# Optimization experiments

Hardware: AMD Instinct MI355X
Metric: run time of the kernel (lower is better)

The kernel has to match this reference:

```python
import jax, jax.numpy as jnp
import numpy as np

D_MODEL = 1024
NUM_HEADS = 16
D_K = D_MODEL // NUM_HEADS
LN_EPS = 1e-5
NEG = -1e9


def setup_inputs() -> dict:
    key = jax.random.key(0)
    ks = jax.random.split(key, 12)
    B, S, D = 8, 1024, D_MODEL
    lim = 1.0 / np.sqrt(D)
    def lin(k):
        k1, k2 = jax.random.split(k)
        W = jax.random.uniform(k1, (D, D), jnp.float32, -lim, lim)
        b = jax.random.uniform(k2, (D,), jnp.float32, -lim, lim)
        return W, b
    Wq, bq = lin(ks[0])
    Wk, bk = lin(ks[1])
    Wv, bv = lin(ks[2])
    Wo, bo = lin(ks[3])
    return {
        "history_items": jax.random.normal(ks[4], (B, S, D), jnp.float32),
        "sequence_mask": jax.random.randint(ks[5], (B, S), 0, 2, jnp.int32),
        "Wq": Wq, "bq": bq, "Wk": Wk, "bk": bk,
        "Wv": Wv, "bv": bv, "Wo": Wo, "bo": bo,
        "ln_gamma": jnp.ones((D,), jnp.float32),
        "ln_beta": jnp.zeros((D,), jnp.float32),
    }


def reference(history_items, sequence_mask, Wq, bq, Wk, bk, Wv, bv, Wo, bo, ln_gamma, ln_beta):
    B, S, D = history_items.shape
    H, dk = NUM_HEADS, D_K
    # projections -> [B, H, S, dk]
    def proj(W, b):
        return (history_items @ W.T + b).reshape(B, S, H, dk).transpose(0, 2, 1, 3)
    q = proj(Wq, bq)
    k = proj(Wk, bk)
    v = proj(Wv, bv)
    # combined mask: causal [1,1,S,S] AND key-padding [B,1,1,S]
    causal = jnp.tril(jnp.ones((S, S), bool))[None, None]
    mask = jnp.logical_and(causal, (sequence_mask != 0)[:, None, None, :])
    scores = jnp.einsum('bhqd,bhkd->bhqk', q, k) / np.sqrt(dk).astype(np.float32)
    scores = jnp.where(mask, scores, NEG)
    attn = jax.nn.softmax(scores, axis=-1)
    ctx = jnp.einsum('bhqk,bhkd->bhqd', attn, v)  # [B,H,S,dk]
    concat = ctx.transpose(0, 2, 1, 3).reshape(B, S, D)
    out = concat @ Wo.T + bo
    x = out + history_items
    mu = jnp.mean(x, axis=-1, keepdims=True)
    var = jnp.mean((x - mu) ** 2, axis=-1, keepdims=True)
    return (x - mu) * jax.lax.rsqrt(var + LN_EPS) * ln_gamma + ln_beta
```

## Files before the change

### kernel.cpp

```cpp
#include <hip/hip_runtime.h>
#include <hip/hip_bf16.h>

#define B_ 8
#define S_ 1024
#define D_ 1024
#define H_ 16
#define DK_ 64
#define M_ (B_*S_)

#define QSCALE 0.1803368801111904f

typedef __attribute__((ext_vector_type(4))) float f32x4;
typedef __attribute__((ext_vector_type(8))) short bf16x8;
typedef __attribute__((ext_vector_type(4))) short s16x4;
typedef __hip_bfloat16 bf16;
typedef unsigned long long ull;

#define GLOAD_LDS16(gp, lp) __builtin_amdgcn_global_load_lds( \
    (const __attribute__((address_space(1))) void*)(gp), \
    (__attribute__((address_space(3))) void*)(lp), 16, 0, 0)

#define SBAR()   asm volatile("s_barrier" ::: "memory")
#define VMCNT(n) asm volatile("s_waitcnt vmcnt(" #n ")" ::: "memory")

__device__ __forceinline__ bf16x8 ld8(const bf16* p){ return *(const bf16x8*)p; }

__device__ __forceinline__ short bf16bits(float f){
  bf16 h = __float2bfloat16(f);
  return __builtin_bit_cast(short, h);
}
__device__ __forceinline__ float tof(short b){
  unsigned u = ((unsigned)(unsigned short)b) << 16;
  return __builtin_bit_cast(float, u);
}

__device__ __forceinline__ bf16x8 ld8swz(const bf16* base, int row, int colb){
  int sw = colb ^ ((row & 7) << 4);
  return *(const bf16x8*)((const char*)base + row*128 + sw);
}

template<int CTRL>
__device__ __forceinline__ float dppadd(float x){
  int m = __builtin_amdgcn_update_dpp(0, __builtin_bit_cast(int,x), CTRL, 0xF, 0xF, true);
  return x + __builtin_bit_cast(float,m);
}
__device__ __forceinline__ float red16add(float x){
  x = dppadd<0xB1>(x);
  x = dppadd<0x4E>(x);
  x = dppadd<0x141>(x);
  x = dppadd<0x140>(x);
  return x;
}

__global__ __launch_bounds__(256) void cast_f32_bf16(const float* __restrict__ in,
                                                     bf16* __restrict__ out, int n){
  int i = (blockIdx.x*256 + threadIdx.x)*8;
  if (i >= n) return;
  f32x4 a = *(const f32x4*)(in+i);
  f32x4 b = *(const f32x4*)(in+i+4);
  bf16x8 o;
  #pragma unroll
  for (int c=0;c<4;c++){ o[c] = bf16bits(a[c]); o[c+4] = bf16bits(b[c]); }
  *(bf16x8*)(out+i) = o;
}

__global__ __launch_bounds__(256) void cast_w4(const float* __restrict__ w0, const float* __restrict__ w1,
                                               const float* __restrict__ w2, const float* __restrict__ w3,
                                               bf16* __restrict__ out){
  int sel = blockIdx.x >> 9;
  const float* src = (sel==0)?w0:((sel==1)?w1:((sel==2)?w2:w3));
  int i = (((blockIdx.x & 511)*256) + threadIdx.x)*8;
  f32x4 a = *(const f32x4*)(src+i);
  f32x4 b = *(const f32x4*)(src+i+4);
  bf16x8 o;
  #pragma unroll
  for (int c=0;c<4;c++){ o[c] = bf16bits(a[c]); o[c+4] = bf16bits(b[c]); }
  *(bf16x8*)(out + ((size_t)sel<<20) + i) = o;
}

__global__ __launch_bounds__(256) void vmean_kernel(const bf16* __restrict__ Vt_g,
                                                    float* __restrict__ vmean){
  int r = blockIdx.x*4 + (threadIdx.x>>6);
  int lane = threadIdx.x & 63;
  const bf16* p = Vt_g + (((size_t)r)<<10) + lane*16;
  bf16x8 a = ld8(p), c = ld8(p+8);
  float s = 0.f;
  #pragma unroll
  for (int e=0;e<8;e++) s += tof(a[e]) + tof(c[e]);
  #pragma unroll
  for (int off=1;off<64;off<<=1) s += __shfl_xor(s, off);
  if (lane==0) vmean[r] = s * (1.f/1024.f);
}

template<int MODE>
__global__ __launch_bounds__(256) void gemm128(
    const bf16* __restrict__ A,
    const bf16* __restrict__ W0, const bf16* __restrict__ W1, const bf16* __restrict__ W2,
    const float* __restrict__ b0, const float* __restrict__ b1, const float* __restrict__ b2,
    bf16* __restrict__ o0, bf16* __restrict__ o1, bf16* __restrict__ o2,
    const float* __restrict__ resid, float* __restrict__ xout)
{
  const bf16* Wsel = W0; const float* bsel = b0;
  if (MODE==0){
    int z = blockIdx.z;
    Wsel = (z==0)?W0:((z==1)?W1:W2);
    bsel = (z==0)?b0:((z==1)?b1:b2);
  }
  __shared__ bf16 smem[4*128*64];
  const int tid = threadIdx.x, wid = tid>>6, lane = tid&63;
  const int lr = lane&15, lg = lane>>4;
  const int m0 = blockIdx.x*128, n0 = blockIdx.y*128;
  const int wr = wid>>1, wc = wid&1;
  f32x4 acc[4][4] = {};

  auto STAGE = [&](int k0, int bsel_){
    #pragma unroll
    for (int c=0;c<4;c++){
      int ldsoff = ((c<<2)|wid)<<10;
      int off = ldsoff + (lane<<4);
      int row = off>>7;
      int colb = (off&127) ^ ((row&7)<<4);
      GLOAD_LDS16(A   + (((size_t)(m0+row))<<10) + k0 + (colb>>1), (char*)smem + bsel_*32768 + ldsoff);
      GLOAD_LDS16(Wsel+ (((size_t)(n0+row))<<10) + k0 + (colb>>1), (char*)smem + bsel_*32768 + 16384 + ldsoff);
    }
  };

  STAGE(0, 0);
  int cur = 0;
  for (int kt=0; kt<16; kt++){
    if (kt < 15){ STAGE((kt+1)<<6, cur^1); VMCNT(8); }
    else        { VMCNT(0); }
    SBAR();
    __builtin_amdgcn_sched_barrier(0);
    const bf16* Asb = smem + cur*16384;
    const bf16* Bsb = Asb + 8192;
    bf16x8 af[4][2], bfv[4][2];
    #pragma unroll
    for (int m=0;m<4;m++){
      int row = wr*64 + m*16 + lr;
      af[m][0] = ld8swz(Asb, row, lg*16);
      af[m][1] = ld8swz(Asb, row, lg*16 + 64);
    }
    #pragma unroll
    for (int n=0;n<4;n++){
      int row = wc*64 + n*16 + lr;
      bfv[n][0] = ld8swz(Bsb, row, lg*16);
      bfv[n][1] = ld8swz(Bsb, row, lg*16 + 64);
    }
    #pragma unroll
    for (int m=0;m<4;m++)
      #pragma unroll
      for (int n=0;n<4;n++){
        acc[m][n] = __builtin_amdgcn_mfma_f32_16x16x32_bf16(af[m][0], bfv[n][0], acc[m][n],0,0,0);
        acc[m][n] = __builtin_amdgcn_mfma_f32_16x16x32_bf16(af[m][1], bfv[n][1], acc[m][n],0,0,0);
      }
    __builtin_amdgcn_sched_barrier(0);
    SBAR();
    cur ^= 1;
  }

  if (MODE==0){
    if (blockIdx.z == 2){
      __syncthreads();
      #pragma unroll
      for (int n=0;n<4;n++){
        int c = wc*64 + n*16 + lr;
        float bias = bsel[n0 + c];
        #pragma unroll
        for (int m=0;m<4;m++){
          int r0 = wr*64 + m*16 + lg*4;
          s16x4 pk;
          #pragma unroll
          for (int j=0;j<4;j++) pk[j] = bf16bits(acc[m][n][j] + bias);
          *(s16x4*)((char*)smem + c*256 + ((r0*2) ^ ((c&7)<<4))) = pk;
        }
      }
      __syncthreads();
      #pragma unroll
      for (int q=0;q<8;q++){
        int idx = tid + q*256;
        int c = idx>>4, r8 = idx&15;
        bf16x8 vv = *(const bf16x8*)((char*)smem + c*256 + ((r8*16) ^ ((c&7)<<4)));
        int col = n0 + c;  int h = col>>6, dd = col&63;
        int row0 = m0 + r8*8;  int bb = row0>>10, s0 = row0&1023;
        *(bf16x8*)(o2 + ((((size_t)bb*H_ + h)*DK_ + dd)<<10) + s0) = vv;
      }
    } else {
      bf16* osel = (blockIdx.z==0) ? o0 : o1;
      const float qs = (blockIdx.z==0) ? QSCALE : 1.0f;
      #pragma unroll
      for (int n=0;n<4;n++){
        int col = n0 + wc*64 + n*16 + lr;
        float bias = bsel[col];
        int h = col>>6, dd = col&63;
        #pragma unroll
        for (int m=0;m<4;m++)
          #pragma unroll
          for (int j=0;j<4;j++){
            int row = m0 + wr*64 + m*16 + lg*4 + j;
            int bb = row>>10, s = row&1023;
            osel[((((size_t)bb*H_ + h)<<10) + s)*DK_ + dd] = __float2bfloat16((acc[m][n][j] + bias)*qs);
          }
      }
    }
  } else {
    #pragma unroll
    for (int n=0;n<4;n++){
      int col = n0 + wc*64 + n*16 + lr;
      float bias = bsel[col];
      #pragma unroll
      for (int m=0;m<4;m++)
        #pragma unroll
        for (int j=0;j<4;j++){
          int row = m0 + wr*64 + m*16 + lg*4 + j;
          size_t idx = (((size_t)row)<<10) + col;
          xout[idx] = acc[m][n][j] + bias + resid[idx];
        }
    }
  }
}

__global__ __launch_bounds__(512) void attn_kernel(
    const bf16* __restrict__ Q, const bf16* __restrict__ K, const bf16* __restrict__ Vt_g,
    const int* __restrict__ seqm, const float* __restrict__ vmean, bf16* __restrict__ ctxout)
{
  __shared__ bf16 Ks[2][64*64];
  __shared__ bf16 Vs[2][64*64];
  __shared__ bf16 Ps[8][32*72];
  __shared__ int msk[1024];
  const int tid = threadIdx.x, wid = tid>>6, lane = tid&63;
  const int lr = lane&15, lg = lane>>4;
  const int bh = blockIdx.x, xb = blockIdx.y;
  const int b = bh>>4, h = bh&15;
  const bf16* Qb  = Q    + (size_t)bh * S_ * DK_;
  const bf16* Kb  = K    + (size_t)bh * S_ * DK_;
  const bf16* Vtb = Vt_g + (size_t)bh * DK_ * S_;
  for (int i=tid;i<1024;i+=512) msk[i] = seqm[b*1024+i];

  const int g0 = 8*xb + wid;
  const int rb0 = g0*16;
  const int rb1 = (63 - g0)*16;
  bf16x8 qf[2][2];
  {
    const bf16* p0 = Qb + (size_t)(rb0+lr)*DK_ + lg*8;
    const bf16* p1 = Qb + (size_t)(rb1+lr)*DK_ + lg*8;
    qf[0][0] = ld8(p0); qf[0][1] = ld8(p0+32);
    qf[1][0] = ld8(p1); qf[1][1] = ld8(p1+32);
  }
  f32x4 cacc[2][4] = {};
  float lsum[2][4] = {};

  auto STAGE = [&](int t, int bsel){
    const int j0 = t*64;
    int off = (wid<<10) + (lane<<4);
    int row = off>>7;
    int colb = (off&127) ^ ((row&7)<<4);
    GLOAD_LDS16(Kb  + (size_t)(j0+row)*DK_ + (colb>>1), (char*)&Ks[bsel][0] + (wid<<10));
    GLOAD_LDS16(Vtb + (((size_t)row)<<10) + j0 + (colb>>1), (char*)&Vs[bsel][0] + (wid<<10));
  };

  STAGE(0, 0);
  __syncthreads();

  ull mbits = 0;
  #pragma unroll
  for (int i=0;i<64;i++) mbits |= ((ull)(msk[i*16+lr]!=0)) << i;

  const int bnt = ((1023 - 128*xb) >> 6) + 1;

  int cur = 0;
  for (int t=0; t<bnt; t++){
    VMCNT(0);
    SBAR();
    if (t+1 < bnt) STAGE(t+1, cur^1);
    const int j0 = t*64;
    if (j0 <= rb1 + 15){
      const bool act0 = (j0 <= rb0 + 15);
      bf16x8 kf[4][2];
      #pragma unroll
      for (int nf=0;nf<4;nf++){
        kf[nf][0] = ld8swz(&Ks[cur][0], nf*16+lr, lg*16);
        kf[nf][1] = ld8swz(&Ks[cur][0], nf*16+lr, lg*16 + 64);
      }
      float madd[4];
      #pragma unroll
      for (int nf=0;nf<4;nf++)
        madd[nf] = ((mbits >> (t*4 + nf)) & 1ull) ? 0.f : -1.0e9f;

      #pragma unroll
      for (int mf=0;mf<2;mf++){
        if (mf==0 && !act0) continue;
        const int rbm = mf ? rb1 : rb0;
        const bool diag = (j0 + 63 > rbm);
        f32x4 sc[4] = {};
        __builtin_amdgcn_s_setprio(1);
        #pragma unroll
        for (int nf=0;nf<4;nf++){
          sc[nf] = __builtin_amdgcn_mfma_f32_16x16x32_bf16(qf[mf][0], kf[nf][0], sc[nf],0,0,0);
          sc[nf] = __builtin_amdgcn_mfma_f32_16x16x32_bf16(qf[mf][1], kf[nf][1], sc[nf],0,0,0);
        }
        __builtin_amdgcn_s_setprio(0);
        #pragma unroll
        for (int j=0;j<4;j++){
          int row = rbm + lg*4 + j;
          float ps = 0.f;
          #pragma unroll
          for (int nf=0;nf<4;nf++){
            float s = sc[nf][j] + madd[nf];
            if (diag){
              int col = j0 + nf*16 + lr;
              s = (col <= row) ? s : -1.0e9f;
            }
            float p = exp2f(s);
            sc[nf][j] = p;
            ps += p;
          }
          lsum[mf][j] += ps;
        }
        #pragma unroll
        for (int nf=0;nf<4;nf++)
          #pragma unroll
          for (int j=0;j<4;j++)
            Ps[wid][(mf*16+lg*4+j)*72 + nf*16+lr] = __float2bfloat16(sc[nf][j]);
      }
      bf16x8 pf[2][2];
      #pragma unroll
      for (int mf=0;mf<2;mf++){
        if (mf==0 && !act0) continue;
        const bf16* p = &Ps[wid][(mf*16+lr)*72 + lg*8];
        pf[mf][0] = *(const bf16x8*)p; pf[mf][1] = *(const bf16x8*)(p+32);
      }
      __builtin_amdgcn_s_setprio(1);
      #pragma unroll
      for (int df=0;df<4;df++){
        #pragma unroll
        for (int kk=0;kk<2;kk++){
          bf16x8 vf = ld8swz(&Vs[cur][0], df*16+lr, lg*16 + kk*64);
          if (act0)
            cacc[0][df] = __builtin_amdgcn_mfma_f32_16x16x32_bf16(pf[0][kk], vf, cacc[0][df],0,0,0);
          cacc[1][df] = __builtin_amdgcn_mfma_f32_16x16x32_bf16(pf[1][kk], vf, cacc[1][df],0,0,0);
        }
      }
      __builtin_amdgcn_s_setprio(0);
    }
    cur ^= 1;
  }

  #pragma unroll
  for (int mf=0;mf<2;mf++){
    const int rbm = mf ? rb1 : rb0;
    float lt[4];
    #pragma unroll
    for (int j=0;j<4;j++) lt[j] = red16add(lsum[mf][j]);
    #pragma unroll
    for (int df=0;df<4;df++)
      #pragma unroll
      for (int j=0;j<4;j++){
        int srow = rbm + lg*4 + j;
        int dd = df*16 + lr;
        float v = cacc[mf][df][j] / lt[j];
        if (lt[j] <= 1.0e-30f) v = vmean[bh*64 + dd];
        ctxout[((size_t)b*S_ + srow)*D_ + h*DK_ + dd] = __float2bfloat16(v);
      }
  }
}

__global__ __launch_bounds__(256) void ln_kernel(const float* __restrict__ X2,
    const float* __restrict__ gamma, const float* __restrict__ beta, float* __restrict__ out)
{
  const int row = blockIdx.x, tid = threadIdx.x;
  const int lane = tid&63, wid = tid>>6;
  const f32x4* xr = (const f32x4*)(X2 + (((size_t)row)<<10));
  f32x4 v = xr[tid];
  float s  = v[0]+v[1]+v[2]+v[3];
  float s2 = v[0]*v[0]+v[1]*v[1]+v[2]*v[2]+v[3]*v[3];
  #pragma unroll
  for (int off=1;off<64;off<<=1){ s += __shfl_xor(s,off); s2 += __shfl_xor(s2,off); }
  __shared__ float red[8];
  if (lane==0){ red[wid]=s; red[wid+4]=s2; }
  __syncthreads();
  s  = red[0]+red[1]+red[2]+red[3];
  s2 = red[4]+red[5]+red[6]+red[7];
  float mu  = s*(1.f/1024.f);
  float var = s2*(1.f/1024.f) - mu*mu;
  float inv = rsqrtf(var + 1e-5f);
  f32x4 gv = ((const f32x4*)gamma)[tid], bv = ((const f32x4*)beta)[tid];
  f32x4 o;
  #pragma unroll
  for (int c=0;c<4;c++) o[c] = (v[c]-mu)*inv*gv[c] + bv[c];
  ((f32x4*)(out + (((size_t)row)<<10)))[tid] = o;
}

extern "C" void kernel_launch(void* const* d_in, const int* in_sizes, int n_in,
                              void* d_out, int out_size, void* d_ws, size_t ws_size,
                              hipStream_t stream) {
  const float* X   = (const float*)d_in[0];
  const int*   sm  = (const int*)d_in[1];
  const float* Wq  = (const float*)d_in[2];  const float* bq = (const float*)d_in[3];
  const float* Wk  = (const float*)d_in[4];  const float* bk = (const float*)d_in[5];
  const float* Wv  = (const float*)d_in[6];  const float* bv = (const float*)d_in[7];
  const float* Wo  = (const float*)d_in[8];  const float* bo = (const float*)d_in[9];
  const float* ga  = (const float*)d_in[10]; const float* be = (const float*)d_in[11];
  float* out = (float*)d_out;
  char* ws = (char*)d_ws;

  bf16* Xbf = (bf16*)(ws);
  bf16* Wqb = (bf16*)(ws + (16u<<20));
  bf16* Wkb = (bf16*)(ws + (18u<<20));
  bf16* Wvb = (bf16*)(ws + (20u<<20));
  bf16* Wob = (bf16*)(ws + (22u<<20));
  bf16* Qh  = (bf16*)(ws + (24u<<20));
  bf16* Kh  = (bf16*)(ws + (40u<<20));
  bf16* Vth = (bf16*)(ws + (56u<<20));
  bf16* Ctx = (bf16*)(ws + (72u<<20));
  float* X2 = (float*)(ws + (24u<<20));
  float* vmean = (float*)(ws + (16u<<20));

  cast_f32_bf16<<<4096,256,0,stream>>>(X,  Xbf, M_*D_);
  cast_w4<<<2048,256,0,stream>>>(Wq, Wk, Wv, Wo, Wqb);

  dim3 g1(M_/128, D_/128, 3);
  gemm128<0><<<g1,256,0,stream>>>(Xbf, Wqb,Wkb,Wvb, bq,bk,bv, Qh,Kh,Vth, nullptr, nullptr);

  vmean_kernel<<<B_*H_*DK_/4,256,0,stream>>>(Vth, vmean);

  dim3 g2(B_*H_, 4);
  attn_kernel<<<g2,512,0,stream>>>(Qh, Kh, Vth, sm, vmean, Ctx);

  dim3 g3(M_/128, D_/128, 1);
  gemm128<1><<<g3,256,0,stream>>>(Ctx, Wob,nullptr,nullptr, bo,nullptr,nullptr,
                                  nullptr,nullptr,nullptr, X, X2);

  ln_kernel<<<M_,256,0,stream>>>(X2, ga, be, out);
}
```

Baseline: 181.9 us.

## Keep attention probabilities in registers via transposed QK MFMA and merge cast kernels

The QK^T MFMA now takes its operands swapped, so each lane holds scores laid out to be packed directly into bf16 A-operand fragments for the PV MFMA. This removes the per-warp LDS round trip for P. To make that work, the V^T write in the QKV GEMM permutes sequence positions within 32-element groups so they match the register order. The key-padding mask is built per tile with a ballot instead of a precomputed 64-bit mask, row sums are reduced with shuffles, and the two cast kernels are merged into one launch. The layout permutation couples the GEMM epilogue to the attention kernel and adds risk of subtle ordering bugs.

Measured after the change: 184.0 us. About the same (+1.1%).

```diff
diff --git a/kernel.cpp b/kernel.cpp
--- a/kernel.cpp
+++ b/kernel.cpp
@@ -33,49 +33,40 @@
   unsigned u = ((unsigned)(unsigned short)b) << 16;
   return __builtin_bit_cast(float, u);
 }
+__device__ __forceinline__ int cvtpk(float a, float b){
+  int r; asm("v_cvt_pk_bf16_f32 %0, %1, %2" : "=v"(r) : "v"(a), "v"(b)); return r;
+}
 
 __device__ __forceinline__ bf16x8 ld8swz(const bf16* base, int row, int colb){
   int sw = colb ^ ((row & 7) << 4);
   return *(const bf16x8*)((const char*)base + row*128 + sw);
 }
 
-template<int CTRL>
-__device__ __forceinline__ float dppadd(float x){
-  int m = __builtin_amdgcn_update_dpp(0, __builtin_bit_cast(int,x), CTRL, 0xF, 0xF, true);
-  return x + __builtin_bit_cast(float,m);
-}
-__device__ __forceinline__ float red16add(float x){
-  x = dppadd<0xB1>(x);
-  x = dppadd<0x4E>(x);
-  x = dppadd<0x141>(x);
-  x = dppadd<0x140>(x);
-  return x;
-}
-
-__global__ __launch_bounds__(256) void cast_f32_bf16(const float* __restrict__ in,
-                                                     bf16* __restrict__ out, int n){
-  int i = (blockIdx.x*256 + threadIdx.x)*8;
-  if (i >= n) return;
-  f32x4 a = *(const f32x4*)(in+i);
-  f32x4 b = *(const f32x4*)(in+i+4);
-  bf16x8 o;
-  #pragma unroll
-  for (int c=0;c<4;c++){ o[c] = bf16bits(a[c]); o[c+4] = bf16bits(b[c]); }
-  *(bf16x8*)(out+i) = o;
-}
-
-__global__ __launch_bounds__(256) void cast_w4(const float* __restrict__ w0, const float* __restrict__ w1,
-                                               const float* __restrict__ w2, const float* __restrict__ w3,
-                                               bf16* __restrict__ out){
-  int sel = blockIdx.x >> 9;
-  const float* src = (sel==0)?w0:((sel==1)?w1:((sel==2)?w2:w3));
-  int i = (((blockIdx.x & 511)*256) + threadIdx.x)*8;
-  f32x4 a = *(const f32x4*)(src+i);
-  f32x4 b = *(const f32x4*)(src+i+4);
-  bf16x8 o;
-  #pragma unroll
-  for (int c=0;c<4;c++){ o[c] = bf16bits(a[c]); o[c+4] = bf16bits(b[c]); }
-  *(bf16x8*)(out + ((size_t)sel<<20) + i) = o;
+__global__ __launch_bounds__(256) void cast_all(const float* __restrict__ X,
+    const float* __restrict__ w0, const float* __restrict__ w1,
+    const float* __restrict__ w2, const float* __restrict__ w3,
+    bf16* __restrict__ Xout, bf16* __restrict__ Wout){
+  int bid = blockIdx.x;
+  if (bid < 4096){
+    int i = (bid*256 + threadIdx.x)*8;
+    f32x4 a = *(const f32x4*)(X+i);
+    f32x4 b = *(const f32x4*)(X+i+4);
+    bf16x8 o;
+    #pragma unroll
+    for (int c=0;c<4;c++){ o[c] = bf16bits(a[c]); o[c+4] = bf16bits(b[c]); }
+    *(bf16x8*)(Xout+i) = o;
+  } else {
+    int bb = bid - 4096;
+    int sel = bb >> 9;
+    const float* src = (sel==0)?w0:((sel==1)?w1:((sel==2)?w2:w3));
+    int i = (((bb & 511)*256) + threadIdx.x)*8;
+    f32x4 a = *(const f32x4*)(src+i);
+    f32x4 b = *(const f32x4*)(src+i+4);
+    bf16x8 o;
+    #pragma unroll
+    for (int c=0;c<4;c++){ o[c] = bf16bits(a[c]); o[c+4] = bf16bits(b[c]); }
+    *(bf16x8*)(Wout + ((size_t)sel<<20) + i) = o;
+  }
 }
 
 __global__ __launch_bounds__(256) void vmean_kernel(const bf16* __restrict__ Vt_g,
@@ -183,7 +174,14 @@
         bf16x8 vv = *(const bf16x8*)((char*)smem + c*256 + ((r8*16) ^ ((c&7)<<4)));
         int col = n0 + c;  int h = col>>6, dd = col&63;
         int row0 = m0 + r8*8;  int bb = row0>>10, s0 = row0&1023;
-        *(bf16x8*)(o2 + ((((size_t)bb*H_ + h)*DK_ + dd)<<10) + s0) = vv;
+        int a = (s0>>3)&3;
+        int O = 16*(a&1) + 4*(a>>1);
+        bf16* dst = o2 + ((((size_t)bb*H_ + h)*DK_ + dd)<<10) + (s0 & ~31) + O;
+        s16x4 lo, hi;
+        lo[0]=vv[0]; lo[1]=vv[1]; lo[2]=vv[2]; lo[3]=vv[3];
+        hi[0]=vv[4]; hi[1]=vv[5]; hi[2]=vv[6]; hi[3]=vv[7];
+        *(s16x4*)dst       = lo;
+        *(s16x4*)(dst + 8) = hi;
       }
     } else {
       bf16* osel = (blockIdx.z==0) ? o0 : o1;
@@ -226,7 +224,6 @@
 {
   __shared__ bf16 Ks[2][64*64];
   __shared__ bf16 Vs[2][64*64];
-  __shared__ bf16 Ps[8][32*72];
   __shared__ int msk[1024];
   const int tid = threadIdx.x, wid = tid>>6, lane = tid&63;
   const int lr = lane&15, lg = lane>>4;
@@ -248,7 +245,7 @@
     qf[1][0] = ld8(p1); qf[1][1] = ld8(p1+32);
   }
   f32x4 cacc[2][4] = {};
-  float lsum[2][4] = {};
+  float lsum[2] = {0.f, 0.f};
 
   auto STAGE = [&](int t, int bsel){
     const int j0 = t*64;
@@ -262,10 +259,6 @@
   STAGE(0, 0);
   __syncthreads();
 
-  ull mbits = 0;
-  #pragma unroll
-  for (int i=0;i<64;i++) mbits |= ((ull)(msk[i*16+lr]!=0)) << i;
-
   const int bnt = ((1023 - 128*xb) >> 6) + 1;
 
   int cur = 0;
@@ -276,70 +269,65 @@
     const int j0 = t*64;
     if (j0 <= rb1 + 15){
       const bool act0 = (j0 <= rb0 + 15);
+      ull bt = __ballot(msk[j0 + lane] != 0);
+      unsigned btl = (unsigned)bt, bth = (unsigned)(bt >> 32);
+
       bf16x8 kf[4][2];
       #pragma unroll
       for (int nf=0;nf<4;nf++){
         kf[nf][0] = ld8swz(&Ks[cur][0], nf*16+lr, lg*16);
         kf[nf][1] = ld8swz(&Ks[cur][0], nf*16+lr, lg*16 + 64);
       }
-      float madd[4];
-      #pragma unroll
-      for (int nf=0;nf<4;nf++)
-        madd[nf] = ((mbits >> (t*4 + nf)) & 1ull) ? 0.f : -1.0e9f;
-
+
+      bf16x8 pf[2][2];
       #pragma unroll
       for (int mf=0;mf<2;mf++){
         if (mf==0 && !act0) continue;
         const int rbm = mf ? rb1 : rb0;
         const bool diag = (j0 + 63 > rbm);
+        const int qrel = rbm + lr - j0;
         f32x4 sc[4] = {};
         __builtin_amdgcn_s_setprio(1);
         #pragma unroll
         for (int nf=0;nf<4;nf++){
-          sc[nf] = __builtin_amdgcn_mfma_f32_16x16x32_bf16(qf[mf][0], kf[nf][0], sc[nf],0,0,0);
-          sc[nf] = __builtin_amdgcn_mfma_f32_16x16x32_bf16(qf[mf][1], kf[nf][1], sc[nf],0,0,0);
+          sc[nf] = __builtin_amdgcn_mfma_f32_16x16x32_bf16(kf[nf][0], qf[mf][0], sc[nf],0,0,0);
+          sc[nf] = __builtin_amdgcn_mfma_f32_16x16x32_bf16(kf[nf][1], qf[mf][1], sc[nf],0,0,0);
         }
         __builtin_amdgcn_s_setprio(0);
+        float ls = 0.f;
         #pragma unroll
-        for (int j=0;j<4;j++){
-          int row = rbm + lg*4 + j;
-          float ps = 0.f;
+        for (int nf=0;nf<4;nf++){
+          unsigned hb2 = (nf<2) ? btl : bth;
           #pragma unroll
-          for (int nf=0;nf<4;nf++){
-            float s = sc[nf][j] + madd[nf];
-            if (diag){
-              int col = j0 + nf*16 + lr;
-              s = (col <= row) ? s : -1.0e9f;
-            }
-            float p = exp2f(s);
+          for (int j=0;j<4;j++){
+            float p = exp2f(sc[nf][j]);
+            bool ok = ((hb2 >> (16*(nf&1) + 4*lg + j)) & 1u) != 0u;
+            if (diag) ok = ok && (16*nf + 4*lg + j <= qrel);
+            p = ok ? p : 0.f;
             sc[nf][j] = p;
-            ps += p;
+            ls += p;
           }
-          lsum[mf][j] += ps;
         }
-        #pragma unroll
-        for (int nf=0;nf<4;nf++)
-          #pragma unroll
-          for (int j=0;j<4;j++)
-            Ps[wid][(mf*16+lg*4+j)*72 + nf*16+lr] = __float2bfloat16(sc[nf][j]);
-      }
-      bf16x8 pf[2][2];
-      #pragma unroll
-      for (int mf=0;mf<2;mf++){
-        if (mf==0 && !act0) continue;
-        const bf16* p = &Ps[wid][(mf*16+lr)*72 + lg*8];
-        pf[mf][0] = *(const bf16x8*)p; pf[mf][1] = *(const bf16x8*)(p+32);
+        lsum[mf] += ls;
+        int4 w0, w1;
+        w0.x = cvtpk(sc[0][0], sc[0][1]); w0.y = cvtpk(sc[0][2], sc[0][3]);
+        w0.z = cvtpk(sc[1][0], sc[1][1]); w0.w = cvtpk(sc[1][2], sc[1][3]);
+        w1.x = cvtpk(sc[2][0], sc[2][1]); w1.y = cvtpk(sc[2][2], sc[2][3]);
+        w1.z = cvtpk(sc[3][0], sc[3][1]); w1.w = cvtpk(sc[3][2], sc[3][3]);
+        pf[mf][0] = __builtin_bit_cast(bf16x8, w0);
+        pf[mf][1] = __builtin_bit_cast(bf16x8, w1);
       }
       __builtin_amdgcn_s_setprio(1);
       #pragma unroll
       for (int df=0;df<4;df++){
-        #pragma unroll
-        for (int kk=0;kk<2;kk++){
-          bf16x8 vf = ld8swz(&Vs[cur][0], df*16+lr, lg*16 + kk*64);
-          if (act0)
-            cacc[0][df] = __builtin_amdgcn_mfma_f32_16x16x32_bf16(pf[0][kk], vf, cacc[0][df],0,0,0);
-          cacc[1][df] = __builtin_amdgcn_mfma_f32_16x16x32_bf16(pf[1][kk], vf, cacc[1][df],0,0,0);
+        bf16x8 vf0 = ld8swz(&Vs[cur][0], df*16+lr, lg*16);
+        bf16x8 vf1 = ld8swz(&Vs[cur][0], df*16+lr, lg*16 + 64);
+        if (act0){
+          cacc[0][df] = __builtin_amdgcn_mfma_f32_16x16x32_bf16(pf[0][0], vf0, cacc[0][df],0,0,0);
+          cacc[0][df] = __builtin_amdgcn_mfma_f32_16x16x32_bf16(pf[0][1], vf1, cacc[0][df],0,0,0);
         }
+        cacc[1][df] = __builtin_amdgcn_mfma_f32_16x16x32_bf16(pf[1][0], vf0, cacc[1][df],0,0,0);
+        cacc[1][df] = __builtin_amdgcn_mfma_f32_16x16x32_bf16(pf[1][1], vf1, cacc[1][df],0,0,0);
       }
       __builtin_amdgcn_s_setprio(0);
     }
@@ -349,17 +337,21 @@
   #pragma unroll
   for (int mf=0;mf<2;mf++){
     const int rbm = mf ? rb1 : rb0;
-    float lt[4];
-    #pragma unroll
-    for (int j=0;j<4;j++) lt[j] = red16add(lsum[mf][j]);
+    float T = lsum[mf];
+    T += __shfl_xor(T, 16);
+    T += __shfl_xor(T, 32);
+    float lden[4];
+    #pragma unroll
+    for (int j=0;j<4;j++)
+      lden[j] = __shfl(T, (lane & 48) | (lg*4 + j));
     #pragma unroll
     for (int df=0;df<4;df++)
       #pragma unroll
       for (int j=0;j<4;j++){
         int srow = rbm + lg*4 + j;
         int dd = df*16 + lr;
-        float v = cacc[mf][df][j] / lt[j];
-        if (lt[j] <= 1.0e-30f) v = vmean[bh*64 + dd];
+        float v = cacc[mf][df][j] / lden[j];
+        if (lden[j] < 1e-30f) v = vmean[bh*64 + dd];
         ctxout[((size_t)b*S_ + srow)*D_ + h*DK_ + dd] = __float2bfloat16(v);
       }
   }
@@ -416,8 +408,7 @@
   float* X2 = (float*)(ws + (24u<<20));
   float* vmean = (float*)(ws + (16u<<20));
 
-  cast_f32_bf16<<<4096,256,0,stream>>>(X,  Xbf, M_*D_);
-  cast_w4<<<2048,256,0,stream>>>(Wq, Wk, Wv, Wo, Wqb);
+  cast_all<<<6144,256,0,stream>>>(X, Wq, Wk, Wv, Wo, Xbf, Wqb);
 
   dim3 g1(M_/128, D_/128, 3);
   gemm128<0><<<g1,256,0,stream>>>(Xbf, Wqb,Wkb,Wvb, bq,bk,bv, Qh,Kh,Vth, nullptr, nullptr);
```

## Fuse casts, compute V means in GEMM epilogue, store residual sum in bf16

Applied to the files above, without the earlier changes.

Merges the input and weight cast kernels into one launch. The separate V-mean kernel is removed: the QKV GEMM epilogue now accumulates per-head column sums into a buffer with atomics, and that buffer is zeroed by the cast kernel and lives in the output buffer as scratch. The pre-LayerNorm residual sum is now stored as bf16 instead of fp32, halving that intermediate's traffic. This cuts two launches and one pass over V, at the cost of atomic contention and reduced precision in the LayerNorm input.

After: 170.6 us. 6.2% less time.

```diff
diff --git a/kernel.cpp b/kernel.cpp
--- a/kernel.cpp
+++ b/kernel.cpp
@@ -52,44 +52,34 @@
   return x;
 }
 
-__global__ __launch_bounds__(256) void cast_f32_bf16(const float* __restrict__ in,
-                                                     bf16* __restrict__ out, int n){
-  int i = (blockIdx.x*256 + threadIdx.x)*8;
-  if (i >= n) return;
-  f32x4 a = *(const f32x4*)(in+i);
-  f32x4 b = *(const f32x4*)(in+i+4);
-  bf16x8 o;
-  #pragma unroll
-  for (int c=0;c<4;c++){ o[c] = bf16bits(a[c]); o[c+4] = bf16bits(b[c]); }
-  *(bf16x8*)(out+i) = o;
-}
-
-__global__ __launch_bounds__(256) void cast_w4(const float* __restrict__ w0, const float* __restrict__ w1,
-                                               const float* __restrict__ w2, const float* __restrict__ w3,
-                                               bf16* __restrict__ out){
-  int sel = blockIdx.x >> 9;
-  const float* src = (sel==0)?w0:((sel==1)?w1:((sel==2)?w2:w3));
-  int i = (((blockIdx.x & 511)*256) + threadIdx.x)*8;
-  f32x4 a = *(const f32x4*)(src+i);
-  f32x4 b = *(const f32x4*)(src+i+4);
-  bf16x8 o;
-  #pragma unroll
-  for (int c=0;c<4;c++){ o[c] = bf16bits(a[c]); o[c+4] = bf16bits(b[c]); }
-  *(bf16x8*)(out + ((size_t)sel<<20) + i) = o;
-}
-
-__global__ __launch_bounds__(256) void vmean_kernel(const bf16* __restrict__ Vt_g,
-                                                    float* __restrict__ vmean){
-  int r = blockIdx.x*4 + (threadIdx.x>>6);
-  int lane = threadIdx.x & 63;
-  const bf16* p = Vt_g + (((size_t)r)<<10) + lane*16;
-  bf16x8 a = ld8(p), c = ld8(p+8);
-  float s = 0.f;
-  #pragma unroll
-  for (int e=0;e<8;e++) s += tof(a[e]) + tof(c[e]);
-  #pragma unroll
-  for (int off=1;off<64;off<<=1) s += __shfl_xor(s, off);
-  if (lane==0) vmean[r] = s * (1.f/1024.f);
+__global__ __launch_bounds__(256) void cast_all(const float* __restrict__ X,
+    const float* __restrict__ w0, const float* __restrict__ w1,
+    const float* __restrict__ w2, const float* __restrict__ w3,
+    bf16* __restrict__ Xout, bf16* __restrict__ Wout, float* __restrict__ vmean){
+  int bid = blockIdx.x;
+  if (bid < 4096){
+    int i = (bid*256 + threadIdx.x)*8;
+    f32x4 a = *(const f32x4*)(X+i);
+    f32x4 b = *(const f32x4*)(X+i+4);
+    bf16x8 o;
+    #pragma unroll
+    for (int c=0;c<4;c++){ o[c] = bf16bits(a[c]); o[c+4] = bf16bits(b[c]); }
+    *(bf16x8*)(Xout+i) = o;
+  } else {
+    int bb = bid - 4096;
+    int sel = bb >> 9;
+    const float* src = (sel==0)?w0:((sel==1)?w1:((sel==2)?w2:w3));
+    int i = (((bb & 511)*256) + threadIdx.x)*8;
+    f32x4 a = *(const f32x4*)(src+i);
+    f32x4 b = *(const f32x4*)(src+i+4);
+    bf16x8 o;
+    #pragma unroll
+    for (int c=0;c<4;c++){ o[c] = bf16bits(a[c]); o[c+4] = bf16bits(b[c]); }
+    *(bf16x8*)(Wout + ((size_t)sel<<20) + i) = o;
+    if (bid == 6143){
+      for (int k=threadIdx.x; k<8192; k+=256) vmean[k] = 0.f;
+    }
+  }
 }
 
 template<int MODE>
@@ -98,7 +88,7 @@
     const bf16* __restrict__ W0, const bf16* __restrict__ W1, const bf16* __restrict__ W2,
     const float* __restrict__ b0, const float* __restrict__ b1, const float* __restrict__ b2,
     bf16* __restrict__ o0, bf16* __restrict__ o1, bf16* __restrict__ o2,
-    const float* __restrict__ resid, float* __restrict__ xout)
+    const float* __restrict__ resid, bf16* __restrict__ x2b, float* __restrict__ vmean)
 {
   const bf16* Wsel = W0; const float* bsel = b0;
   if (MODE==0){
@@ -161,6 +151,23 @@
 
   if (MODE==0){
     if (blockIdx.z == 2){
+      const int b = m0 >> 10;
+      #pragma unroll
+      for (int n=0;n<4;n++){
+        int col = n0 + wc*64 + n*16 + lr;
+        float bias = bsel[col];
+        float s = 16.f * bias;
+        #pragma unroll
+        for (int m=0;m<4;m++)
+          #pragma unroll
+          for (int j=0;j<4;j++) s += acc[m][n][j];
+        s += __shfl_xor(s, 16);
+        s += __shfl_xor(s, 32);
+        if (lg == 0){
+          int h = col>>6, dd = col&63;
+          atomicAdd(vmean + ((b*H_ + h)<<6) + dd, s);
+        }
+      }
       __syncthreads();
       #pragma unroll
       for (int n=0;n<4;n++){
@@ -207,14 +214,14 @@
     #pragma unroll
     for (int n=0;n<4;n++){
       int col = n0 + wc*64 + n*16 + lr;
-      float bias = bsel[col];
+      float bias = b0[col];
       #pragma unroll
       for (int m=0;m<4;m++)
         #pragma unroll
         for (int j=0;j<4;j++){
           int row = m0 + wr*64 + m*16 + lg*4 + j;
           size_t idx = (((size_t)row)<<10) + col;
-          xout[idx] = acc[m][n][j] + bias + resid[idx];
+          x2b[idx] = __float2bfloat16(acc[m][n][j] + bias + resid[idx]);
         }
     }
   }
@@ -359,19 +366,22 @@
         int srow = rbm + lg*4 + j;
         int dd = df*16 + lr;
         float v = cacc[mf][df][j] / lt[j];
-        if (lt[j] <= 1.0e-30f) v = vmean[bh*64 + dd];
+        if (lt[j] <= 1.0e-30f) v = vmean[bh*64 + dd] * (1.f/1024.f);
         ctxout[((size_t)b*S_ + srow)*D_ + h*DK_ + dd] = __float2bfloat16(v);
       }
   }
 }
 
-__global__ __launch_bounds__(256) void ln_kernel(const float* __restrict__ X2,
+__global__ __launch_bounds__(256) void ln_kernel(const bf16* __restrict__ X2,
     const float* __restrict__ gamma, const float* __restrict__ beta, float* __restrict__ out)
 {
   const int row = blockIdx.x, tid = threadIdx.x;
   const int lane = tid&63, wid = tid>>6;
-  const f32x4* xr = (const f32x4*)(X2 + (((size_t)row)<<10));
-  f32x4 v = xr[tid];
+  const s16x4* xr = (const s16x4*)(X2 + (((size_t)row)<<10));
+  s16x4 xv = xr[tid];
+  f32x4 v;
+  #pragma unroll
+  for (int c=0;c<4;c++) v[c] = tof(xv[c]);
   float s  = v[0]+v[1]+v[2]+v[3];
   float s2 = v[0]*v[0]+v[1]*v[1]+v[2]*v[2]+v[3]*v[3];
   #pragma unroll
@@ -413,23 +423,21 @@
   bf16* Kh  = (bf16*)(ws + (40u<<20));
   bf16* Vth = (bf16*)(ws + (56u<<20));
   bf16* Ctx = (bf16*)(ws + (72u<<20));
-  float* X2 = (float*)(ws + (24u<<20));
-  float* vmean = (float*)(ws + (16u<<20));
-
-  cast_f32_bf16<<<4096,256,0,stream>>>(X,  Xbf, M_*D_);
-  cast_w4<<<2048,256,0,stream>>>(Wq, Wk, Wv, Wo, Wqb);
+  bf16* X2b = (bf16*)(ws + (24u<<20));
+  float* vmean = (float*)d_out;
+
+  cast_all<<<6144,256,0,stream>>>(X, Wq, Wk, Wv, Wo, Xbf, Wqb, vmean);
 
   dim3 g1(M_/128, D_/128, 3);
-  gemm128<0><<<g1,256,0,stream>>>(Xbf, Wqb,Wkb,Wvb, bq,bk,bv, Qh,Kh,Vth, nullptr, nullptr);
-
-  vmean_kernel<<<B_*H_*DK_/4,256,0,stream>>>(Vth, vmean);
+  gemm128<0><<<g1,256,0,stream>>>(Xbf, Wqb,Wkb,Wvb, bq,bk,bv, Qh,Kh,Vth,
+                                  nullptr, nullptr, vmean);
 
   dim3 g2(B_*H_, 4);
   attn_kernel<<<g2,512,0,stream>>>(Qh, Kh, Vth, sm, vmean, Ctx);
 
   dim3 g3(M_/128, D_/128, 1);
   gemm128<1><<<g3,256,0,stream>>>(Ctx, Wob,nullptr,nullptr, bo,nullptr,nullptr,
-                                  nullptr,nullptr,nullptr, X, X2);
-
-  ln_kernel<<<M_,256,0,stream>>>(X2, ga, be, out);
-}
+                                  nullptr,nullptr,nullptr, X, X2b, nullptr);
+
+  ln_kernel<<<M_,256,0,stream>>>(X2b, ga, be, out);
+}
```
